# Kernel optimization log

Measured on AMD Instinct MI355X. Metric: run time of the kernel, lower is better.

Reference implementation:

```python
import jax, jax.numpy as jnp
import numpy as np

N = 64
NUM_INPUTS = 6
NUM_OUTPUTS = 2
T_STEPS = 1024
BATCH = 1024
DT = 1.0
TAU = 10.0
ALPHA = DT / TAU
SIGMA_REC = 0.03
SIGMA_INP = 0.03
SLOPE = 1.0  # activation_slope for relu


def setup_inputs() -> dict:
    key = jax.random.key(0)
    k_u, k_rn, k_in, k_wi, k_wr, k_wo = jax.random.split(key, 6)
    u = jax.random.normal(k_u, (NUM_INPUTS, T_STEPS, BATCH), dtype=jnp.float32)
    rec_noise = jax.random.normal(k_rn, (N, T_STEPS, BATCH), dtype=jnp.float32)
    inp_noise = jax.random.normal(k_in, (NUM_INPUTS, T_STEPS, BATCH), dtype=jnp.float32)
    # learned params (masks are all-ones, already folded in)
    W_inp = jax.random.normal(k_wi, (N, NUM_INPUTS), dtype=jnp.float32) * 0.3
    W_rec = jax.random.normal(k_wr, (N, N), dtype=jnp.float32) * (0.9 / np.sqrt(N))
    W_out = jax.random.normal(k_wo, (NUM_OUTPUTS, N), dtype=jnp.float32) * 0.3
    return {"u": u, "rec_noise": rec_noise, "inp_noise": inp_noise,
            "W_inp": W_inp, "W_rec": W_rec, "W_out": W_out}


def _forward(u, rec_noise, inp_noise, W_inp, W_rec, W_out):
    # scale standard-normal noise exactly as torch: sqrt(2/alpha * sigma^2) * randn
    rn = jnp.sqrt(2.0 / ALPHA) * SIGMA_REC * rec_noise   # (N, T, B)
    inn = jnp.sqrt(2.0 / ALPHA) * SIGMA_INP * inp_noise  # (num_inputs, T, B)
    # move to (T, B, feat) for scan
    u_t = jnp.transpose(u, (1, 2, 0))     # (T, B, num_inputs)
    rn_t = jnp.transpose(rn, (1, 2, 0))   # (T, B, N)
    inn_t = jnp.transpose(inn, (1, 2, 0)) # (T, B, num_inputs)
    x0 = jnp.zeros((BATCH, N), dtype=u.dtype)  # self.x = zeros(N), broadcast over batch

    def step(x, inp):
        u_i, rn_i, in_i = inp
        pre = x @ W_rec.T + (u_i + in_i) @ W_inp.T
        act = jnp.maximum(0.0, SLOPE * pre)
        x_new = (1.0 - ALPHA) * x + ALPHA * (act + rn_i)
        return x_new, x_new

    # the torch loop runs T_steps-1 iterations using inputs at steps 0..T-2
    _, xs = jax.lax.scan(step, x0, (u_t[:-1], rn_t[:-1], inn_t[:-1]))
    states_tbn = jnp.concatenate([x0[None], xs], axis=0)  # (T, B, N)
    outputs_tbo = states_tbn @ W_out.T                    # (T, B, num_outputs)
    states = jnp.transpose(states_tbn, (2, 0, 1))   # (N, T, B)
    outputs = jnp.transpose(outputs_tbo, (2, 0, 1)) # (num_outputs, T, B)
    return states, outputs


def reference(u, rec_noise, inp_noise, W_inp, W_rec, W_out):
    return _forward(u, rec_noise, inp_noise, W_inp, W_rec, W_out)
```

## Files before the change

kernel.cpp:

```cpp
#include <hip/hip_runtime.h>

#define NN 64
#define NI 6
#define TT 1024
#define BB 1024
#define TB (TT * BB)
#define NSCALE 0.13416407864998738f
#define ARNSCALE 0.013416407864998739f
#define RREC 72
#define BSTRIDE (TT * RREC)

typedef __attribute__((ext_vector_type(2))) unsigned int u32x2;

__device__ __forceinline__ float rdlane(float v, int l) {
    return __int_as_float(__builtin_amdgcn_readlane(__float_as_int(v), l));
}

__global__ __launch_bounds__(256) void build_rnu(
    const float* __restrict__ u,
    const float* __restrict__ rn,
    const float* __restrict__ inn,
    float* __restrict__ rnu)
{
    const int blk = blockIdx.x;
    const int t   = blk >> 4;
    const int b0  = (blk & 15) * 64;
    const int tid = threadIdx.x;

    __shared__ float lds[64][65];

    {
        const int c  = tid & 63;
        const int r0 = tid >> 6;
#pragma unroll
        for (int it = 0; it < 16; ++it) {
            const int n = 4 * it + r0;
            lds[c][n] = ARNSCALE * rn[n * TB + t * BB + b0 + c];
        }
    }
    __syncthreads();
    {
        const int cn = tid & 63;
        const int r0 = tid >> 6;
#pragma unroll
        for (int it = 0; it < 16; ++it) {
            const int r = 4 * it + r0;
            rnu[(b0 + r) * BSTRIDE + t * RREC + cn] = lds[r][cn];
        }
    }
    {
        const int i  = tid & 7;
        const int br = tid >> 3;
#pragma unroll
        for (int it = 0; it < 2; ++it) {
            const int b = br + 32 * it;
            float v = 0.0f;
            if (i < NI) {
                const int g = i * TB + t * BB + b0 + b;
                v = fmaf(NSCALE, inn[g], u[g]);
            }
            rnu[(b0 + b) * BSTRIDE + t * RREC + 64 + i] = v;
        }
    }
}

__global__ __launch_bounds__(64, 1) void latent_rnn_hp(
    const float* __restrict__ rn_in,
    float* __restrict__ x_out,
    const float* __restrict__ Winp,
    const float* __restrict__ Wrec)
{
    const int hw = blockIdx.x;
    const int b  = (hw & 7) * 128 + (hw >> 3);
    const int n  = threadIdx.x;
    const int h  = n >> 5;
    const int hb = 32 * h;
    const int np = n ^ 32;

    __shared__ __align__(16) float xs[2][64];

    float ws[32], wp[32];
#pragma unroll
    for (int j = 0; j < 32; j += 4) {
        const float4 a = *reinterpret_cast<const float4*>(Wrec + n  * NN + hb + j);
        const float4 c = *reinterpret_cast<const float4*>(Wrec + np * NN + hb + j);
        ws[j] = a.x; ws[j+1] = a.y; ws[j+2] = a.z; ws[j+3] = a.w;
        wp[j] = c.x; wp[j+1] = c.y; wp[j+2] = c.z; wp[j+3] = c.w;
    }
    float wi[NI];
#pragma unroll
    for (int i = 0; i < NI; ++i) wi[i] = Winp[n * NI + i];
#pragma unroll
    for (int k = 0; k < 32; ++k) { asm volatile("" : "+v"(ws[k])); asm volatile("" : "+v"(wp[k])); }

    bool useX;
    {
        u32x2 pb = __builtin_amdgcn_permlane32_swap((unsigned)n, (unsigned)n, false, false);
        useX = (pb.x == (unsigned)np);
    }

    const float* rptr = rn_in + b * BSTRIDE + n;
    const float* uptr = rn_in + b * BSTRIDE + 64 + (n & 7);
    float*       xdst = x_out + b * BSTRIDE + n;

    xs[0][n] = 0.0f;

    float rnb[4], utb[4];
#pragma unroll
    for (int d = 0; d < 4; ++d) {
        rnb[d] = rptr[d * RREC];
        utb[d] = uptr[d * RREC];
    }

    float xreg = 0.0f;

#define STEP_BODY(tcur, slot, P, TPEXPR)                                      \
    do {                                                                      \
        const float rcur = rnb[slot];                                         \
        const float ucur = utb[slot];                                         \
        { const int tp = (TPEXPR);                                            \
          rnb[slot] = rptr[tp * RREC];                                        \
          utb[slot] = uptr[tp * RREC]; }                                      \
           \
        float a0 = rdlane(ucur, 0) * wi[0];                                   \
        float a1 = rdlane(ucur, 1) * wi[1];                                   \
        a0 = fmaf(rdlane(ucur, 2), wi[2], a0);                                \
        a1 = fmaf(rdlane(ucur, 3), wi[3], a1);                                \
        a0 = fmaf(rdlane(ucur, 4), wi[4], a0);                                \
        a1 = fmaf(rdlane(ucur, 5), wi[5], a1);                                \
        \
        const float4* xrow = reinterpret_cast<const float4*>(&xs[P][hb]);     \
        float c0 = 0.f, c1 = 0.f;                                             \
        _Pragma("unroll")                                                     \
        for (int q = 0; q < 8; ++q) {                                         \
            const float4 v = xrow[q];                                         \
            a0 = fmaf(v.x, ws[4*q+0], a0); c0 = fmaf(v.x, wp[4*q+0], c0);     \
            a1 = fmaf(v.y, ws[4*q+1], a1); c1 = fmaf(v.y, wp[4*q+1], c1);     \
            a0 = fmaf(v.z, ws[4*q+2], a0); c0 = fmaf(v.z, wp[4*q+2], c0);     \
            a1 = fmaf(v.w, ws[4*q+3], a1); c1 = fmaf(v.w, wp[4*q+3], c1);     \
        }                                                                     \
          \
        const float p2 = c0 + c1;                                             \
        u32x2 sw = __builtin_amdgcn_permlane32_swap(                          \
            __float_as_uint(p2), __float_as_uint(p2), false, false);          \
        const float pr = __uint_as_float(useX ? sw.x : sw.y);                 \
        const float pre = (a0 + a1) + pr;                                     \
        const float xn  = fmaf(0.9f, xreg,                                    \
                               fmaf(0.1f, fmaxf(pre, 0.f), rcur));            \
        xreg = xn;                                                            \
        xs[(P) ^ 1][n] = xn;                        \
        xdst[(tcur) * RREC] = xn;                    \
    } while (0)

#define STEP_NC(tcur, slot, P) STEP_BODY(tcur, slot, P, (tcur) + 4)
#define STEP_CL(tcur, slot, P) \
    STEP_BODY(tcur, slot, P, ((tcur) + 4 < TT - 1) ? (tcur) + 4 : TT - 1)

#pragma unroll 1
    for (int t = 0; t < 1020; t += 4) {
        STEP_NC(t + 0, 0, 0);
        STEP_NC(t + 1, 1, 1);
        STEP_NC(t + 2, 2, 0);
        STEP_NC(t + 3, 3, 1);
    }
    STEP_CL(1020, 0, 0);
    STEP_CL(1021, 1, 1);
    STEP_CL(1022, 2, 0);
#undef STEP_NC
#undef STEP_CL
#undef STEP_BODY
}

__global__ __launch_bounds__(256) void trans_out(
    const float* __restrict__ rnu,
    const float* __restrict__ Wout,
    float* __restrict__ states,
    float* __restrict__ outputs)
{
    const int blk = blockIdx.x;
    const int t   = blk >> 4;
    const int b0  = (blk & 15) * 64;
    const int tid = threadIdx.x;

    __shared__ float xt[64][65];
    __shared__ float wo[2][64];

    if (tid < 128) wo[tid >> 6][tid & 63] = Wout[tid];

    const int col = tid & 63;
    const int r0  = tid >> 6;
    if (t == 0) {
#pragma unroll
        for (int it = 0; it < 16; ++it) xt[4 * it + r0][col] = 0.0f;
    } else {
#pragma unroll
        for (int it = 0; it < 16; ++it) {
            const int r = 4 * it + r0;
            xt[r][col] = rnu[(b0 + r) * BSTRIDE + (t - 1) * RREC + col];
        }
    }
    __syncthreads();

#pragma unroll
    for (int it = 0; it < 16; ++it) {
        const int n = 4 * it + r0;
        states[n * TB + t * BB + b0 + col] = xt[col][n];
    }

    if (tid < 128) {
        const int o  = tid >> 6;
        const int bb = tid & 63;
        float acc = 0.0f;
#pragma unroll
        for (int k = 0; k < NN; ++k) acc = fmaf(xt[bb][k], wo[o][k], acc);
        outputs[o * TB + t * BB + b0 + bb] = acc;
    }
}

#define BARRIER() do {                                                        \
    __builtin_amdgcn_sched_barrier(0);                                        \
    asm volatile("s_waitcnt lgkmcnt(0)\n\ts_barrier" ::: "memory");           \
    __builtin_amdgcn_sched_barrier(0);                                        \
} while (0)

__global__ __launch_bounds__(256, 1) void latent_rnn_fb(
    const float* __restrict__ u, const float* __restrict__ rn,
    const float* __restrict__ inn, const float* __restrict__ Winp,
    const float* __restrict__ Wrec, float* __restrict__ states)
{
    const int hw  = blockIdx.x;
    const int lb  = (hw & 7) * 32 + (hw >> 3);
    const int b0  = lb * 4;
    const int tid = threadIdx.x;
    const int l   = tid & 63;
    const int w   = tid >> 6;
    const int n   = tid >> 2;
    const int bs  = tid & 3;

    __shared__ float rnT[2][NN][5];
    __shared__ float xT[2][NN][5];
    __shared__ float iT[2][4][8];

    float wreg[NN];
#pragma unroll
    for (int k = 0; k < NN; k += 4) {
        const float4 w4 = *reinterpret_cast<const float4*>(Wrec + l * NN + k);
        wreg[k] = w4.x; wreg[k+1] = w4.y; wreg[k+2] = w4.z; wreg[k+3] = w4.w;
    }
    float wi[NI];
#pragma unroll
    for (int i = 0; i < NI; ++i) wi[i] = Winp[l * NI + i];

    const float* rsrc = rn + n * TB + b0 + bs;
    float*       sdst = states + n * TB + b0 + bs;
    const bool  ist  = (tid < NI * 4);
    const int   ii   = tid >> 2;
    const int   ib   = tid & 3;
    const float* usrc = u   + ii * TB + b0 + ib;
    const float* isrc = inn + ii * TB + b0 + ib;

    rnT[0][n][bs] = rsrc[0];
    if (ist) iT[0][ib][ii] = fmaf(NSCALE, isrc[0], usrc[0]);
    xT[0][l][w] = 0.0f;

    float rnPF[4], uPF[4], iPF[4];
#pragma unroll
    for (int d = 0; d < 4; ++d) {
        rnPF[d] = rsrc[(d + 1) * BB];
        if (ist) { uPF[d] = usrc[(d + 1) * BB]; iPF[d] = isrc[(d + 1) * BB]; }
    }
    __syncthreads();

    float xreg = 0.0f;

#define FSTEP(tcur, slot, CC)                                                 \
  {                                                                           \
    sdst[(tcur) * BB] = xT[CC][n][bs];                                        \
    const float rcur = rnT[CC][l][w];                                         \
    const float4 iv0 = *reinterpret_cast<const float4*>(&iT[CC][w][0]);       \
    const float2 iv1 = *reinterpret_cast<const float2*>(&iT[CC][w][4]);       \
    float a0 = 0.f, a1 = 0.f, a2 = 0.f, a3 = 0.f;                             \
    _Pragma("unroll")                                                         \
    for (int k = 0; k < NN; k += 4) {                                         \
        a0 = fmaf(rdlane(xreg, k + 0), wreg[k + 0], a0);                      \
        a1 = fmaf(rdlane(xreg, k + 1), wreg[k + 1], a1);                      \
        a2 = fmaf(rdlane(xreg, k + 2), wreg[k + 2], a2);                      \
        a3 = fmaf(rdlane(xreg, k + 3), wreg[k + 3], a3);                      \
    }                                                                         \
    a0 = fmaf(iv0.x, wi[0], a0); a1 = fmaf(iv0.y, wi[1], a1);                 \
    a2 = fmaf(iv0.z, wi[2], a2); a3 = fmaf(iv0.w, wi[3], a3);                 \
    a0 = fmaf(iv1.x, wi[4], a0); a1 = fmaf(iv1.y, wi[5], a1);                 \
    const float pre = (a0 + a1) + (a2 + a3);                                  \
    const float xn  = fmaf(0.9f, xreg,                                        \
                           fmaf(0.1f, fmaxf(pre, 0.f), ARNSCALE * rcur));     \
    xreg = xn;                                                                \
    xT[(CC) ^ 1][l][w] = xn;                                                  \
    rnT[(CC) ^ 1][n][bs] = rnPF[slot];                                        \
    if (ist) iT[(CC) ^ 1][ib][ii] = fmaf(NSCALE, iPF[slot], uPF[slot]);       \
    { int tp = (tcur) + 5; if (tp > TT - 2) tp = TT - 2;                      \
      rnPF[slot] = rsrc[tp * BB];                                             \
      if (ist) { uPF[slot] = usrc[tp * BB]; iPF[slot] = isrc[tp * BB]; } }    \
    BARRIER();                                                                \
  }

#pragma unroll 1
    for (int t = 0; t < 1020; t += 4) {
        FSTEP(t + 0, 0, 0);
        FSTEP(t + 1, 1, 1);
        FSTEP(t + 2, 2, 0);
        FSTEP(t + 3, 3, 1);
    }
    FSTEP(1020, 0, 0);
    FSTEP(1021, 1, 1);
    FSTEP(1022, 2, 0);
#undef FSTEP

    sdst[(TT - 1) * BB] = xT[1][n][bs];
}

__global__ __launch_bounds__(256) void out_proj(
    const float* __restrict__ states,
    const float* __restrict__ Wout,
    float* __restrict__ outputs)
{
    const int g4 = (blockIdx.x * 256 + threadIdx.x) * 4;
    float4 a0 = {0.f, 0.f, 0.f, 0.f};
    float4 a1 = {0.f, 0.f, 0.f, 0.f};
#pragma unroll
    for (int k = 0; k < NN; ++k) {
        const float4 s = *reinterpret_cast<const float4*>(states + k * TB + g4);
        const float w0 = Wout[k];
        const float w1 = Wout[NN + k];
        a0.x = fmaf(s.x, w0, a0.x); a0.y = fmaf(s.y, w0, a0.y);
        a0.z = fmaf(s.z, w0, a0.z); a0.w = fmaf(s.w, w0, a0.w);
        a1.x = fmaf(s.x, w1, a1.x); a1.y = fmaf(s.y, w1, a1.y);
        a1.z = fmaf(s.z, w1, a1.z); a1.w = fmaf(s.w, w1, a1.w);
    }
    *reinterpret_cast<float4*>(outputs + g4)      = a0;
    *reinterpret_cast<float4*>(outputs + TB + g4) = a1;
}

extern "C" void kernel_launch(void* const* d_in, const int* in_sizes, int n_in,
                              void* d_out, int out_size, void* d_ws, size_t ws_size,
                              hipStream_t stream) {
    const float* u    = (const float*)d_in[0];
    const float* rn   = (const float*)d_in[1];
    const float* inn  = (const float*)d_in[2];
    const float* Winp = (const float*)d_in[3];
    const float* Wrec = (const float*)d_in[4];
    const float* Wout = (const float*)d_in[5];

    float* states  = (float*)d_out;
    float* outputs = (float*)d_out + (size_t)NN * TT * BB;

    const size_t need = (size_t)BB * TT * RREC * sizeof(float);
    if (ws_size >= need) {
        float* rnu = (float*)d_ws;
        build_rnu<<<TT * 16, 256, 0, stream>>>(u, rn, inn, rnu);
        latent_rnn_hp<<<1024, 64, 0, stream>>>(rnu, rnu, Winp, Wrec);
        trans_out<<<TT * 16, 256, 0, stream>>>(rnu, Wout, states, outputs);
    } else {
        latent_rnn_fb<<<256, 256, 0, stream>>>(u, rn, inn, Winp, Wrec, states);
        out_proj<<<1024, 256, 0, stream>>>(states, Wout, outputs);
    }
}
```

Baseline: 628.8 us.

## Replace LDS state exchange with DPP row-rotate and permlane swaps in RNN step

The recurrent step no longer writes the hidden state to shared memory and reads it back as float4 rows. Each lane now fetches the other lanes' state values with permlane32/permlane16 swaps and DPP row-rotates inside a 16-lane row. The W_rec weights are preloaded in a lane-specific rotated order so every lane's FMAs line up with the rotated values. This removes LDS traffic and its latency from the serial critical path, at the cost of relying on a runtime-detected DPP rotate direction and many cross-lane ops per step.

Result: slower. 993.3 us (+58.0%).

```diff
diff --git a/kernel.cpp b/kernel.cpp
--- a/kernel.cpp
+++ b/kernel.cpp
@@ -15,6 +15,18 @@
 __device__ __forceinline__ float rdlane(float v, int l) {
     return __int_as_float(__builtin_amdgcn_readlane(__float_as_int(v), l));
 }
+
+template<int J>
+__device__ __forceinline__ float rorj(float v) {
+    return __int_as_float(__builtin_amdgcn_update_dpp(
+        __float_as_int(v), __float_as_int(v), 0x120 + J, 0xF, 0xF, false));
+}
+
+#if defined(__has_builtin)
+# if __has_builtin(__builtin_amdgcn_permlane16_swap)
+#  define HAVE_PL16 1
+# endif
+#endif
 
 __global__ __launch_bounds__(256) void build_rnu(
     const float* __restrict__ u,
@@ -29,8 +41,7 @@
 
     __shared__ float lds[64][65];
 
-    {
-        const int c  = tid & 63;
+    {   const int c  = tid & 63;
         const int r0 = tid >> 6;
 #pragma unroll
         for (int it = 0; it < 16; ++it) {
@@ -39,8 +50,7 @@
         }
     }
     __syncthreads();
-    {
-        const int cn = tid & 63;
+    {   const int cn = tid & 63;
         const int r0 = tid >> 6;
 #pragma unroll
         for (int it = 0; it < 16; ++it) {
@@ -48,8 +58,7 @@
             rnu[(b0 + r) * BSTRIDE + t * RREC + cn] = lds[r][cn];
         }
     }
-    {
-        const int i  = tid & 7;
+    {   const int i  = tid & 7;
         const int br = tid >> 3;
 #pragma unroll
         for (int it = 0; it < 2; ++it) {
@@ -64,7 +73,7 @@
     }
 }
 
-__global__ __launch_bounds__(64, 1) void latent_rnn_hp(
+__global__ __launch_bounds__(64, 1) void latent_rnn_dppb(
     const float* __restrict__ rn_in,
     float* __restrict__ x_out,
     const float* __restrict__ Winp,
@@ -73,102 +82,142 @@
     const int hw = blockIdx.x;
     const int b  = (hw & 7) * 128 + (hw >> 3);
     const int n  = threadIdx.x;
-    const int h  = n >> 5;
-    const int hb = 32 * h;
-    const int np = n ^ 32;
-
-    __shared__ __align__(16) float xs[2][64];
-
-    float ws[32], wp[32];
-#pragma unroll
-    for (int j = 0; j < 32; j += 4) {
-        const float4 a = *reinterpret_cast<const float4*>(Wrec + n  * NN + hb + j);
-        const float4 c = *reinterpret_cast<const float4*>(Wrec + np * NN + hb + j);
-        ws[j] = a.x; ws[j+1] = a.y; ws[j+2] = a.z; ws[j+3] = a.w;
-        wp[j] = c.x; wp[j+1] = c.y; wp[j+2] = c.z; wp[j+3] = c.w;
-    }
-    float wi[NI];
-#pragma unroll
-    for (int i = 0; i < NI; ++i) wi[i] = Winp[n * NI + i];
-#pragma unroll
-    for (int k = 0; k < 32; ++k) { asm volatile("" : "+v"(ws[k])); asm volatile("" : "+v"(wp[k])); }
-
-    bool useX;
+
+    int d;
+    {
+        int pr = __builtin_amdgcn_update_dpp(n, n, 0x121, 0xF, 0xF, false);
+        d = __builtin_amdgcn_readfirstlane(pr) & 15;
+    }
+
+    bool useX32;
     {
         u32x2 pb = __builtin_amdgcn_permlane32_swap((unsigned)n, (unsigned)n, false, false);
-        useX = (pb.x == (unsigned)np);
+        useX32 = (pb.x == (unsigned)(n ^ 32));
+    }
+#ifdef HAVE_PL16
+    bool useX16;
+    {
+        u32x2 pb = __builtin_amdgcn_permlane16_swap((unsigned)n, (unsigned)n, false, false);
+        useX16 = (pb.x == (unsigned)(n ^ 16));
+    }
+#endif
+
+    float wr0[16], wr1[16], wr2[16], wr3[16];
+#pragma unroll
+    for (int j = 0; j < 16; ++j) {
+        const int k15 = (n + d * j) & 15;
+        const int kb  = (n & 48) | k15;
+        wr0[j] = Wrec[n * NN + (kb ^  0)];
+        wr1[j] = Wrec[n * NN + (kb ^ 16)];
+        wr2[j] = Wrec[n * NN + (kb ^ 32)];
+        wr3[j] = Wrec[n * NN + (kb ^ 48)];
+    }
+    float wi[NI];
+#pragma unroll
+    for (int i = 0; i < NI; ++i) wi[i] = Winp[n * NI + i];
+#pragma unroll
+    for (int j = 0; j < 16; ++j) {
+        asm volatile("" : "+v"(wr0[j])); asm volatile("" : "+v"(wr1[j]));
+        asm volatile("" : "+v"(wr2[j])); asm volatile("" : "+v"(wr3[j]));
     }
 
     const float* rptr = rn_in + b * BSTRIDE + n;
     const float* uptr = rn_in + b * BSTRIDE + 64 + (n & 7);
     float*       xdst = x_out + b * BSTRIDE + n;
 
-    xs[0][n] = 0.0f;
-
     float rnb[4], utb[4];
 #pragma unroll
-    for (int d = 0; d < 4; ++d) {
-        rnb[d] = rptr[d * RREC];
-        utb[d] = uptr[d * RREC];
+    for (int dd = 0; dd < 4; ++dd) {
+        rnb[dd] = rptr[dd * RREC];
+        utb[dd] = uptr[dd * RREC];
     }
 
     float xreg = 0.0f;
 
-#define STEP_BODY(tcur, slot, P, TPEXPR)                                      \
+#define ROW(J)                                                                \
+    do {                                                                      \
+        const float y0 = rorj<J>(xg0);                                        \
+        const float y1 = rorj<J>(xg1);                                        \
+        const float y2 = rorj<J>(xg2);                                        \
+        const float y3 = rorj<J>(xg3);                                        \
+        p[(4*(J) + 0) & 7] = fmaf(y0, wr0[J], p[(4*(J) + 0) & 7]);            \
+        p[(4*(J) + 1) & 7] = fmaf(y1, wr1[J], p[(4*(J) + 1) & 7]);            \
+        p[(4*(J) + 2) & 7] = fmaf(y2, wr2[J], p[(4*(J) + 2) & 7]);            \
+        p[(4*(J) + 3) & 7] = fmaf(y3, wr3[J], p[(4*(J) + 3) & 7]);            \
+    } while (0)
+
+#define STEP_BODY(tcur, slot, TPEXPR)                                         \
     do {                                                                      \
         const float rcur = rnb[slot];                                         \
         const float ucur = utb[slot];                                         \
         { const int tp = (TPEXPR);                                            \
           rnb[slot] = rptr[tp * RREC];                                        \
           utb[slot] = uptr[tp * RREC]; }                                      \
-           \
-        float a0 = rdlane(ucur, 0) * wi[0];                                   \
-        float a1 = rdlane(ucur, 1) * wi[1];                                   \
-        a0 = fmaf(rdlane(ucur, 2), wi[2], a0);                                \
-        a1 = fmaf(rdlane(ucur, 3), wi[3], a1);                                \
-        a0 = fmaf(rdlane(ucur, 4), wi[4], a0);                                \
-        a1 = fmaf(rdlane(ucur, 5), wi[5], a1);                                \
         \
-        const float4* xrow = reinterpret_cast<const float4*>(&xs[P][hb]);     \
-        float c0 = 0.f, c1 = 0.f;                                             \
-        _Pragma("unroll")                                                     \
-        for (int q = 0; q < 8; ++q) {                                         \
-            const float4 v = xrow[q];                                         \
-            a0 = fmaf(v.x, ws[4*q+0], a0); c0 = fmaf(v.x, wp[4*q+0], c0);     \
-            a1 = fmaf(v.y, ws[4*q+1], a1); c1 = fmaf(v.y, wp[4*q+1], c1);     \
-            a0 = fmaf(v.z, ws[4*q+2], a0); c0 = fmaf(v.z, wp[4*q+2], c0);     \
-            a1 = fmaf(v.w, ws[4*q+3], a1); c1 = fmaf(v.w, wp[4*q+3], c1);     \
+        const float xg0 = xreg;                                               \
+        float xg2, xg1, xg3;                                                  \
+        {                                                                     \
+            u32x2 s = __builtin_amdgcn_permlane32_swap(                       \
+                __float_as_uint(xg0), __float_as_uint(xg0), false, false);    \
+            xg2 = __uint_as_float(useX32 ? s.x : s.y);                        \
         }                                                                     \
-          \
-        const float p2 = c0 + c1;                                             \
-        u32x2 sw = __builtin_amdgcn_permlane32_swap(                          \
-            __float_as_uint(p2), __float_as_uint(p2), false, false);          \
-        const float pr = __uint_as_float(useX ? sw.x : sw.y);                 \
-        const float pre = (a0 + a1) + pr;                                     \
+        SWAP16(xg1, xg0);                                                     \
+        SWAP16(xg3, xg2);                                                     \
+                             \
+        float p[8];                                                           \
+        p[0] = rdlane(ucur, 0) * wi[0];                                       \
+        p[1] = rdlane(ucur, 1) * wi[1];                                       \
+        p[2] = rdlane(ucur, 2) * wi[2];                                       \
+        p[3] = rdlane(ucur, 3) * wi[3];                                       \
+        p[4] = rdlane(ucur, 4) * wi[4];                                       \
+        p[5] = rdlane(ucur, 5) * wi[5];                                       \
+        p[6] = 0.0f; p[7] = 0.0f;                                             \
+                                                  \
+        p[0] = fmaf(xg0, wr0[0], p[0]);                                       \
+        p[1] = fmaf(xg1, wr1[0], p[1]);                                       \
+        p[2] = fmaf(xg2, wr2[0], p[2]);                                       \
+        p[3] = fmaf(xg3, wr3[0], p[3]);                                       \
+        ROW(1);  ROW(2);  ROW(3);  ROW(4);  ROW(5);                           \
+        ROW(6);  ROW(7);  ROW(8);  ROW(9);  ROW(10);                          \
+        ROW(11); ROW(12); ROW(13); ROW(14); ROW(15);                          \
+        const float pre = ((p[0] + p[1]) + (p[2] + p[3])) +                   \
+                          ((p[4] + p[5]) + (p[6] + p[7]));                    \
         const float xn  = fmaf(0.9f, xreg,                                    \
                                fmaf(0.1f, fmaxf(pre, 0.f), rcur));            \
         xreg = xn;                                                            \
-        xs[(P) ^ 1][n] = xn;                        \
         xdst[(tcur) * RREC] = xn;                    \
     } while (0)
 
-#define STEP_NC(tcur, slot, P) STEP_BODY(tcur, slot, P, (tcur) + 4)
-#define STEP_CL(tcur, slot, P) \
-    STEP_BODY(tcur, slot, P, ((tcur) + 4 < TT - 1) ? (tcur) + 4 : TT - 1)
+#ifdef HAVE_PL16
+#define SWAP16(dst, src)                                                      \
+    {                                                                         \
+        u32x2 s = __builtin_amdgcn_permlane16_swap(                           \
+            __float_as_uint(src), __float_as_uint(src), false, false);        \
+        dst = __uint_as_float(useX16 ? s.x : s.y);                            \
+    }
+#else
+#define SWAP16(dst, src) dst = __shfl_xor((src), 16);
+#endif
+
+#define STEP_NC(tcur, slot) STEP_BODY(tcur, slot, (tcur) + 4)
+#define STEP_CL(tcur, slot) \
+    STEP_BODY(tcur, slot, ((tcur) + 4 < TT - 1) ? (tcur) + 4 : TT - 1)
 
 #pragma unroll 1
     for (int t = 0; t < 1020; t += 4) {
-        STEP_NC(t + 0, 0, 0);
-        STEP_NC(t + 1, 1, 1);
-        STEP_NC(t + 2, 2, 0);
-        STEP_NC(t + 3, 3, 1);
-    }
-    STEP_CL(1020, 0, 0);
-    STEP_CL(1021, 1, 1);
-    STEP_CL(1022, 2, 0);
+        STEP_NC(t + 0, 0);
+        STEP_NC(t + 1, 1);
+        STEP_NC(t + 2, 2);
+        STEP_NC(t + 3, 3);
+    }
+    STEP_CL(1020, 0);
+    STEP_CL(1021, 1);
+    STEP_CL(1022, 2);
 #undef STEP_NC
 #undef STEP_CL
 #undef STEP_BODY
+#undef SWAP16
+#undef ROW
 }
 
 __global__ __launch_bounds__(256) void trans_out(
@@ -265,9 +314,9 @@
 
     float rnPF[4], uPF[4], iPF[4];
 #pragma unroll
-    for (int d = 0; d < 4; ++d) {
-        rnPF[d] = rsrc[(d + 1) * BB];
-        if (ist) { uPF[d] = usrc[(d + 1) * BB]; iPF[d] = isrc[(d + 1) * BB]; }
+    for (int dd = 0; dd < 4; ++dd) {
+        rnPF[dd] = rsrc[(dd + 1) * BB];
+        if (ist) { uPF[dd] = usrc[(dd + 1) * BB]; iPF[dd] = isrc[(dd + 1) * BB]; }
     }
     __syncthreads();
 
@@ -357,7 +406,7 @@
     if (ws_size >= need) {
         float* rnu = (float*)d_ws;
         build_rnu<<<TT * 16, 256, 0, stream>>>(u, rn, inn, rnu);
-        latent_rnn_hp<<<1024, 64, 0, stream>>>(rnu, rnu, Winp, Wrec);
+        latent_rnn_dppb<<<1024, 64, 0, stream>>>(rnu, rnu, Winp, Wrec);
         trans_out<<<TT * 16, 256, 0, stream>>>(rnu, Wout, states, outputs);
     } else {
         latent_rnn_fb<<<256, 256, 0, stream>>>(u, rn, inn, Winp, Wrec, states);
```

## Interleave two independent batch recurrences per wavefront in latent RNN kernel

Applied to the files above, without the earlier changes.

Each 64-thread block now advances two batch elements' recurrences together, interleaving their instruction streams so one chain's dependent FMA, LDS and permlane work can hide the other's latency. The grid halves from 1024 to 512 blocks, so fewer wavefronts run on the GPU but each has about twice the instruction-level parallelism. The cost is more registers and a doubled per-step instruction count, which could lengthen the serial critical path if the latency hiding is not enough to offset it.

Result: slower. 746.4 us (+18.7%).

```diff
diff --git a/kernel.cpp b/kernel.cpp
--- a/kernel.cpp
+++ b/kernel.cpp
@@ -29,8 +29,7 @@
 
     __shared__ float lds[64][65];
 
-    {
-        const int c  = tid & 63;
+    {   const int c  = tid & 63;
         const int r0 = tid >> 6;
 #pragma unroll
         for (int it = 0; it < 16; ++it) {
@@ -39,8 +38,7 @@
         }
     }
     __syncthreads();
-    {
-        const int cn = tid & 63;
+    {   const int cn = tid & 63;
         const int r0 = tid >> 6;
 #pragma unroll
         for (int it = 0; it < 16; ++it) {
@@ -48,8 +46,7 @@
             rnu[(b0 + r) * BSTRIDE + t * RREC + cn] = lds[r][cn];
         }
     }
-    {
-        const int i  = tid & 7;
+    {   const int i  = tid & 7;
         const int br = tid >> 3;
 #pragma unroll
         for (int it = 0; it < 2; ++it) {
@@ -64,20 +61,22 @@
     }
 }
 
-__global__ __launch_bounds__(64, 1) void latent_rnn_hp(
+__global__ __launch_bounds__(64, 1) void latent_rnn_2x(
     const float* __restrict__ rn_in,
     float* __restrict__ x_out,
     const float* __restrict__ Winp,
     const float* __restrict__ Wrec)
 {
     const int hw = blockIdx.x;
-    const int b  = (hw & 7) * 128 + (hw >> 3);
+    const int g  = (hw & 7) * 64 + (hw >> 3);
+    const int bA = 2 * g;
+    const int bB = 2 * g + 1;
     const int n  = threadIdx.x;
     const int h  = n >> 5;
     const int hb = 32 * h;
     const int np = n ^ 32;
 
-    __shared__ __align__(16) float xs[2][64];
+    __shared__ __align__(16) float xs[2][2][64];
 
     float ws[32], wp[32];
 #pragma unroll
@@ -99,57 +98,70 @@
         useX = (pb.x == (unsigned)np);
     }
 
-    const float* rptr = rn_in + b * BSTRIDE + n;
-    const float* uptr = rn_in + b * BSTRIDE + 64 + (n & 7);
-    float*       xdst = x_out + b * BSTRIDE + n;
-
-    xs[0][n] = 0.0f;
-
-    float rnb[4], utb[4];
+    const float* rptrA = rn_in + bA * BSTRIDE + n;
+    const float* uptrA = rn_in + bA * BSTRIDE + 64 + (n & 7);
+    float*       xdstA = x_out + bA * BSTRIDE + n;
+    const float* rptrB = rn_in + bB * BSTRIDE + n;
+    const float* uptrB = rn_in + bB * BSTRIDE + 64 + (n & 7);
+    float*       xdstB = x_out + bB * BSTRIDE + n;
+
+    xs[0][0][n] = 0.0f;
+    xs[1][0][n] = 0.0f;
+
+    float rnbA[4], utbA[4], rnbB[4], utbB[4];
 #pragma unroll
     for (int d = 0; d < 4; ++d) {
-        rnb[d] = rptr[d * RREC];
-        utb[d] = uptr[d * RREC];
-    }
-
-    float xreg = 0.0f;
-
-#define STEP_BODY(tcur, slot, P, TPEXPR)                                      \
-    do {                                                                      \
-        const float rcur = rnb[slot];                                         \
-        const float ucur = utb[slot];                                         \
-        { const int tp = (TPEXPR);                                            \
-          rnb[slot] = rptr[tp * RREC];                                        \
-          utb[slot] = uptr[tp * RREC]; }                                      \
-           \
-        float a0 = rdlane(ucur, 0) * wi[0];                                   \
-        float a1 = rdlane(ucur, 1) * wi[1];                                   \
-        a0 = fmaf(rdlane(ucur, 2), wi[2], a0);                                \
-        a1 = fmaf(rdlane(ucur, 3), wi[3], a1);                                \
-        a0 = fmaf(rdlane(ucur, 4), wi[4], a0);                                \
-        a1 = fmaf(rdlane(ucur, 5), wi[5], a1);                                \
-        \
-        const float4* xrow = reinterpret_cast<const float4*>(&xs[P][hb]);     \
-        float c0 = 0.f, c1 = 0.f;                                             \
+        rnbA[d] = rptrA[d * RREC];
+        utbA[d] = uptrA[d * RREC];
+        rnbB[d] = rptrB[d * RREC];
+        utbB[d] = uptrB[d * RREC];
+    }
+
+    float xregA = 0.0f, xregB = 0.0f;
+
+#define CHAIN(S, XS, RNB, UTB, RPTR, UPTR, XDST, XREG, P, TP)                 \
+        const float rcur##S = RNB[slot];                                      \
+        const float ucur##S = UTB[slot];                                      \
+        RNB[slot] = RPTR[(TP) * RREC];                                        \
+        UTB[slot] = UPTR[(TP) * RREC];                                        \
+        float a0##S = rdlane(ucur##S, 0) * wi[0];                             \
+        float a1##S = rdlane(ucur##S, 1) * wi[1];                             \
+        a0##S = fmaf(rdlane(ucur##S, 2), wi[2], a0##S);                       \
+        a1##S = fmaf(rdlane(ucur##S, 3), wi[3], a1##S);                       \
+        a0##S = fmaf(rdlane(ucur##S, 4), wi[4], a0##S);                       \
+        a1##S = fmaf(rdlane(ucur##S, 5), wi[5], a1##S);                       \
+        const float4* xrow##S = reinterpret_cast<const float4*>(&XS[P][hb]);  \
+        float c0##S = 0.f, c1##S = 0.f;                                       \
         _Pragma("unroll")                                                     \
         for (int q = 0; q < 8; ++q) {                                         \
-            const float4 v = xrow[q];                                         \
-            a0 = fmaf(v.x, ws[4*q+0], a0); c0 = fmaf(v.x, wp[4*q+0], c0);     \
-            a1 = fmaf(v.y, ws[4*q+1], a1); c1 = fmaf(v.y, wp[4*q+1], c1);     \
-            a0 = fmaf(v.z, ws[4*q+2], a0); c0 = fmaf(v.z, wp[4*q+2], c0);     \
-            a1 = fmaf(v.w, ws[4*q+3], a1); c1 = fmaf(v.w, wp[4*q+3], c1);     \
+            const float4 v = xrow##S[q];                                      \
+            a0##S = fmaf(v.x, ws[4*q+0], a0##S);                              \
+            c0##S = fmaf(v.x, wp[4*q+0], c0##S);                              \
+            a1##S = fmaf(v.y, ws[4*q+1], a1##S);                              \
+            c1##S = fmaf(v.y, wp[4*q+1], c1##S);                              \
+            a0##S = fmaf(v.z, ws[4*q+2], a0##S);                              \
+            c0##S = fmaf(v.z, wp[4*q+2], c0##S);                              \
+            a1##S = fmaf(v.w, ws[4*q+3], a1##S);                              \
+            c1##S = fmaf(v.w, wp[4*q+3], c1##S);                              \
         }                                                                     \
-          \
-        const float p2 = c0 + c1;                                             \
-        u32x2 sw = __builtin_amdgcn_permlane32_swap(                          \
-            __float_as_uint(p2), __float_as_uint(p2), false, false);          \
-        const float pr = __uint_as_float(useX ? sw.x : sw.y);                 \
-        const float pre = (a0 + a1) + pr;                                     \
-        const float xn  = fmaf(0.9f, xreg,                                    \
-                               fmaf(0.1f, fmaxf(pre, 0.f), rcur));            \
-        xreg = xn;                                                            \
-        xs[(P) ^ 1][n] = xn;                        \
-        xdst[(tcur) * RREC] = xn;                    \
+        const float p2##S = c0##S + c1##S;                                    \
+        u32x2 sw##S = __builtin_amdgcn_permlane32_swap(                       \
+            __float_as_uint(p2##S), __float_as_uint(p2##S), false, false);    \
+        const float pr##S = __uint_as_float(useX ? sw##S.x : sw##S.y);        \
+        const float pre##S = (a0##S + a1##S) + pr##S;                         \
+        const float xn##S = fmaf(0.9f, XREG,                                  \
+                                 fmaf(0.1f, fmaxf(pre##S, 0.f), rcur##S));    \
+        XREG = xn##S;                                                         \
+        XS[(P) ^ 1][n] = xn##S;                                               \
+        XDST[(tcur) * RREC] = xn##S;
+
+#define STEP_BODY(TCUR, SLOT, P, TPEXPR)                                      \
+    do {                                                                      \
+        const int tcur = (TCUR);                                              \
+        const int slot = (SLOT);                                              \
+        const int tp   = (TPEXPR);                                            \
+        CHAIN(A, xs[0], rnbA, utbA, rptrA, uptrA, xdstA, xregA, P, tp)        \
+        CHAIN(B, xs[1], rnbB, utbB, rptrB, uptrB, xdstB, xregB, P, tp)        \
     } while (0)
 
 #define STEP_NC(tcur, slot, P) STEP_BODY(tcur, slot, P, (tcur) + 4)
@@ -169,6 +181,7 @@
 #undef STEP_NC
 #undef STEP_CL
 #undef STEP_BODY
+#undef CHAIN
 }
 
 __global__ __launch_bounds__(256) void trans_out(
@@ -265,9 +278,9 @@
 
     float rnPF[4], uPF[4], iPF[4];
 #pragma unroll
-    for (int d = 0; d < 4; ++d) {
-        rnPF[d] = rsrc[(d + 1) * BB];
-        if (ist) { uPF[d] = usrc[(d + 1) * BB]; iPF[d] = isrc[(d + 1) * BB]; }
+    for (int dd = 0; dd < 4; ++dd) {
+        rnPF[dd] = rsrc[(dd + 1) * BB];
+        if (ist) { uPF[dd] = usrc[(dd + 1) * BB]; iPF[dd] = isrc[(dd + 1) * BB]; }
     }
     __syncthreads();
 
@@ -357,7 +370,7 @@
     if (ws_size >= need) {
         float* rnu = (float*)d_ws;
         build_rnu<<<TT * 16, 256, 0, stream>>>(u, rn, inn, rnu);
-        latent_rnn_hp<<<1024, 64, 0, stream>>>(rnu, rnu, Winp, Wrec);
+        latent_rnn_2x<<<512, 64, 0, stream>>>(rnu, rnu, Winp, Wrec);
         trans_out<<<TT * 16, 256, 0, stream>>>(rnu, Wout, states, outputs);
     } else {
         latent_rnn_fb<<<256, 256, 0, stream>>>(u, rn, inn, Winp, Wrec, states);
```
